# Performance work log

Measured on AMD Instinct MI355X. Metric: run time of the kernel, lower is better.

Reference implementation:

```python
import jax, jax.numpy as jnp
import numpy as np

B, N, D, H = 4, 2048, 768, 12
HD = D // H
SCALE = HD ** -0.5


def setup_inputs() -> dict:
    key = jax.random.key(0)
    k1, k2, k3 = jax.random.split(key, 3)
    x = jax.random.normal(k1, (B, N, D), dtype=jnp.float32)
    w_qkv = jax.random.normal(k2, (D, 3 * D), dtype=jnp.float32) * (D ** -0.5)
    w_proj = jax.random.normal(k3, (D, D), dtype=jnp.float32) * (D ** -0.5)
    b_proj = jnp.zeros((D,), dtype=jnp.float32)
    return {"x": x, "w_qkv": w_qkv, "w_proj": w_proj, "b_proj": b_proj}


def reference(x, w_qkv, w_proj, b_proj):
    b, n, d = x.shape
    qkv = x @ w_qkv                      # [b, n, 3d]
    q, k, v = jnp.split(qkv, 3, axis=-1)
    # [b, n, d] -> [b, h, n, hd]
    split_heads = lambda t: t.reshape(b, n, H, HD).transpose(0, 2, 1, 3)
    q, k, v = split_heads(q), split_heads(k), split_heads(v)
    dots = jnp.einsum('bhqd,bhkd->bhqk', q, k) * SCALE   # [b, h, n, n]
    attn = jax.nn.softmax(dots, axis=-1)
    q_attn = attn[:, :, 0, :]            # attention row of query token 0: [b, h, n]
    # dropout p=0 (eval) -> identity
    out = jnp.einsum('bhqk,bhkd->bhqd', attn, v)          # [b, h, n, hd]
    out = out.transpose(0, 2, 1, 3).reshape(b, n, d)      # [b, n, d]
    return out @ w_proj + b_proj, q_attn
```

## Files before the change

kernel.cpp:

```cpp
#include <hip/hip_runtime.h>


typedef unsigned short u16;
typedef __attribute__((ext_vector_type(8))) short bf8;
typedef __attribute__((ext_vector_type(4))) short bf4;
typedef __attribute__((ext_vector_type(4))) int i4;
typedef __attribute__((ext_vector_type(4))) float f4;

#define MFMA16(a, b, c) __builtin_amdgcn_mfma_f32_16x16x32_bf16((a), (b), (c), 0, 0, 0)

#if __has_builtin(__builtin_amdgcn_exp2f)
#define EXP2(x) __builtin_amdgcn_exp2f(x)
#else
#define EXP2(x) __expf((x) * 0.6931471805599453f)
#endif

__device__ __forceinline__ float b2f(u16 h) {
  union { unsigned u; float f; } v; v.u = ((unsigned)h) << 16; return v.f;
}
__device__ __forceinline__ u16 f2b(float f) {
  union { float f; unsigned u; } v; v.f = f;
  unsigned r = v.u + 0x7fffu + ((v.u >> 16) & 1u);
  return (u16)(r >> 16);
}
__device__ __forceinline__ unsigned pack2(float a, float b) {
#if __has_builtin(__builtin_amdgcn_perm)
  return __builtin_amdgcn_perm(__builtin_bit_cast(unsigned, b),
                               __builtin_bit_cast(unsigned, a), 0x07060302u);
#else
  return (__builtin_bit_cast(unsigned, b) & 0xFFFF0000u) |
         (__builtin_bit_cast(unsigned, a) >> 16);
#endif
}
__device__ __forceinline__ void gload16(const u16* g, u16* l) {
  __builtin_amdgcn_global_load_lds(
      (const __attribute__((address_space(1))) void*)g,
      (__attribute__((address_space(3))) void*)l, 16, 0, 0);
}
__device__ __forceinline__ int detect_f32(const u16* x) {
  unsigned v = x[2 * (threadIdx.x & 63)];
  unsigned e = (v >> 7) & 0xFF;
  return __ballot(e >= 0x8E) != 0ull;
}

__global__ __launch_bounds__(256) void prep(
    const void* __restrict__ x, u16* __restrict__ xbf,
    const void* __restrict__ wqkv, u16* __restrict__ wqkvT,
    const void* __restrict__ wproj, u16* __restrict__ wprojT) {
  const int z = blockIdx.z;
  if (z == 2) {
    const int f32 = detect_f32((const u16*)x);
    const int lin = blockIdx.y * 72 + blockIdx.x;
    if (f32) {
      const float2* in = (const float2*)x;
      unsigned* out = (unsigned*)xbf;
      for (int i = lin * 256 + threadIdx.x; i < 3145728; i += 442368) {
        float2 v = in[i];
        out[i] = (unsigned)f2b(v.x) | ((unsigned)f2b(v.y) << 16);
      }
    } else {
      const unsigned* in = (const unsigned*)x;
      unsigned* out = (unsigned*)xbf;
      for (int i = lin * 256 + threadIdx.x; i < 3145728; i += 442368)
        out[i] = in[i];
    }
    return;
  }
  if (z == 1 && blockIdx.x >= 24) return;
  const void* in = z ? wproj : wqkv;
  u16* out = z ? wprojT : wqkvT;
  const int R = 768, C = z ? 768 : 2304;
  __shared__ u16 tile[32][33];
  const int f32 = detect_f32((const u16*)x);
  const int bx = blockIdx.x * 32, by = blockIdx.y * 32;
  const int tx = threadIdx.x & 31, ty = threadIdx.x >> 5;
#pragma unroll
  for (int i = 0; i < 4; i++) {
    size_t idx = (size_t)(by + ty + i * 8) * C + bx + tx;
    tile[ty + i * 8][tx] = f32 ? f2b(((const float*)in)[idx]) : ((const u16*)in)[idx];
  }
  __syncthreads();
#pragma unroll
  for (int i = 0; i < 4; i++)
    out[(size_t)(bx + ty + i * 8) * R + by + tx] = tile[tx][ty + i * 8];
}

template <int BIAS, int QATTN>
__global__ __launch_bounds__(256, 4) void gemm_bt(
    const u16* __restrict__ A, const u16* __restrict__ Bt,
    const void* __restrict__ bias, void* __restrict__ C,
    int M, int Ncols, int K, const u16* __restrict__ xdet,
    u16* __restrict__ Vt, const float* __restrict__ qe,
    const float* __restrict__ lout) {
  if (QATTN && blockIdx.x == 6) {
    const int f32o = detect_f32(xdet);
    const int base = blockIdx.y * 1536;
    for (int j = threadIdx.x; j < 1536; j += 256) {
      int idx = base + j;
      float v = qe[idx] * (1.f / lout[idx >> 11]);
      size_t oidx = (size_t)6291456 + idx;
      if (f32o) ((float*)C)[oidx] = v; else ((u16*)C)[oidx] = f2b(v);
    }
    return;
  }
  __shared__ alignas(16) u16 Al[2][128 * 32];
  __shared__ alignas(16) u16 Bl[2][128 * 32];
  const int t = threadIdx.x;
  const int lane = t & 63, wave = t >> 6;
  const int wr = wave >> 1, wc = wave & 1;
  const int quad = lane >> 4, l16 = lane & 15;
  const int bm = blockIdx.y * 128, bn = blockIdx.x * 128;
  const int f32o = BIAS ? detect_f32(xdet) : 0;
  const int grow = lane >> 2, gcol = (lane & 3) * 8;
  const int chunk0 = wave * 2, chunk1 = wave * 2 + 1;
  const int arow0 = chunk0 * 16 + grow, arow1 = chunk1 * 16 + grow;
  f4 acc[4][4] = {};
  gload16(A + (size_t)(bm + arow0) * K + gcol, &Al[0][chunk0 * 512]);
  gload16(Bt + (size_t)(bn + arow0) * K + gcol, &Bl[0][chunk0 * 512]);
  gload16(A + (size_t)(bm + arow1) * K + gcol, &Al[0][chunk1 * 512]);
  gload16(Bt + (size_t)(bn + arow1) * K + gcol, &Bl[0][chunk1 * 512]);
  const int NIT = K >> 5;
  for (int i = 0; i < NIT; i++) {
    const int cur = i & 1, nxt = cur ^ 1;
    __syncthreads();
    if (i + 1 < NIT) {
      int k0 = (i + 1) << 5;
      gload16(A + (size_t)(bm + arow0) * K + k0 + gcol, &Al[nxt][chunk0 * 512]);
      gload16(Bt + (size_t)(bn + arow0) * K + k0 + gcol, &Bl[nxt][chunk0 * 512]);
      gload16(A + (size_t)(bm + arow1) * K + k0 + gcol, &Al[nxt][chunk1 * 512]);
      gload16(Bt + (size_t)(bn + arow1) * K + k0 + gcol, &Bl[nxt][chunk1 * 512]);
    }
    bf8 af[4], bfr[4];
#pragma unroll
    for (int mt = 0; mt < 4; mt++)
      af[mt] = *(const bf8*)&Al[cur][(wr * 64 + mt * 16 + l16) * 32 + quad * 8];
#pragma unroll
    for (int nt = 0; nt < 4; nt++)
      bfr[nt] = *(const bf8*)&Bl[cur][(wc * 64 + nt * 16 + l16) * 32 + quad * 8];
#pragma unroll
    for (int mt = 0; mt < 4; mt++)
#pragma unroll
      for (int nt = 0; nt < 4; nt++)
        acc[mt][nt] = MFMA16(af[mt], bfr[nt], acc[mt][nt]);
  }
  if (Vt != nullptr && bn >= 1536) {
    const int b = bm >> 11;
#pragma unroll
    for (int mt = 0; mt < 4; mt++) {
      int n0 = (bm & 2047) + wr * 64 + mt * 16 + quad * 4;
      int n2 = (n0 & ~31) | (((n0 >> 2) & 3) << 3) | (((n0 >> 4) & 1) << 2);
#pragma unroll
      for (int nt = 0; nt < 4; nt++) {
        int colv = bn - 1536 + wc * 64 + nt * 16 + l16;
        int h = colv >> 6, d = colv & 63;
        bf4 pk = {(short)f2b(acc[mt][nt][0]), (short)f2b(acc[mt][nt][1]),
                  (short)f2b(acc[mt][nt][2]), (short)f2b(acc[mt][nt][3])};
        *(bf4*)&Vt[(size_t)((b * 12 + h) * 64 + d) * 2048 + n2] = pk;
      }
    }
    return;
  }
#pragma unroll
  for (int mt = 0; mt < 4; mt++) {
    int row = bm + wr * 64 + mt * 16 + quad * 4;
#pragma unroll
    for (int nt = 0; nt < 4; nt++) {
      int col = bn + wc * 64 + nt * 16 + l16;
      float bv = 0.f;
      if (BIAS)
        bv = f32o ? ((const float*)bias)[col] : b2f(((const u16*)bias)[col]);
#pragma unroll
      for (int r = 0; r < 4; r++) {
        size_t idx = (size_t)(row + r) * Ncols + col;
        float v = acc[mt][nt][r] + bv;
        if (f32o) ((float*)C)[idx] = v; else ((u16*)C)[idx] = f2b(v);
      }
    }
  }
}

__global__ __launch_bounds__(256, 3) void flash_attn(
    const u16* __restrict__ qkv, const u16* __restrict__ Vt,
    u16* __restrict__ O, float* __restrict__ qe, float* __restrict__ lout) {
  __shared__ alignas(16) u16 lds[2][8192];
  const int t = threadIdx.x, lane = t & 63, wave = t >> 6;
  const int quad = lane >> 4, l16 = lane & 15;
  const int id = blockIdx.x;
  const int bh = (id & 7) + 8 * (id >> 7);
  const int qtile = (id >> 3) & 15;
  const int b = bh / 12, h = bh - b * 12;
  const int q0 = qtile * 128 + wave * 32;
  const bool dumpP = (qe != nullptr) && (qtile == 0) && (wave == 0);
  const float SCALE2 = 0.125f * 1.44269504089f;
  const float mM0 = -16.f;
  bf8 qf[2][2];
#pragma unroll
  for (int qt = 0; qt < 2; qt++) {
    const u16* Qr = qkv + (size_t)(b * 2048 + q0 + qt * 16 + l16) * 2304 + h * 64;
    bf8 r0 = *(const bf8*)(Qr + quad * 8);
    bf8 r1 = *(const bf8*)(Qr + 32 + quad * 8);
#pragma unroll
    for (int j = 0; j < 8; j++) {
      qf[qt][0][j] = (short)f2b(b2f((u16)r0[j]) * SCALE2);
      qf[qt][1][j] = (short)f2b(b2f((u16)r1[j]) * SCALE2);
    }
  }
  const u16* Kb = qkv + (size_t)(b * 2048) * 2304 + 768 + h * 64;
  const u16* Vb = Vt + (size_t)((b * 12 + h) * 64) * 2048;
  const int drow = wave * 16 + (lane >> 2);
  const int dcol = ((lane & 3) ^ ((lane >> 3) & 3)) * 8;
  const int swz = (quad ^ ((l16 >> 1) & 3)) * 8;
  f4 o[2][4] = {};
  float lpart[2] = {0.f, 0.f};

  {
    const u16* Kt = Kb + (size_t)drow * 2304 + dcol;
    const u16* Vr = Vb + (size_t)drow * 2048 + dcol;
    u16* base = &lds[0][wave * 512];
    gload16(Kt, base);
    gload16(Kt + 32, base + 2048);
    gload16(Vr, base + 4096);
    gload16(Vr + 32, base + 6144);
  }

  for (int i = 0; i < 32; i++) {
    const int cur = i & 1;
    __syncthreads();
    if (i + 1 < 32) {
      int n1 = (i + 1) * 64;
      const u16* Kt = Kb + (size_t)(n1 + drow) * 2304 + dcol;
      const u16* Vr = Vb + (size_t)drow * 2048 + n1 + dcol;
      u16* base = &lds[cur ^ 1][wave * 512];
      gload16(Kt, base);
      gload16(Kt + 32, base + 2048);
      gload16(Vr, base + 4096);
      gload16(Vr + 32, base + 6144);
    }
    const u16* K0 = &lds[cur][0];
    const u16* K1 = &lds[cur][2048];
    union { i4 i; bf8 b; } pf[2][2];
#pragma unroll
    for (int kt = 0; kt < 4; kt++) {
      bf8 kf0 = *(const bf8*)&K0[(kt * 16 + l16) * 32 + swz];
      bf8 kf1 = *(const bf8*)&K1[(kt * 16 + l16) * 32 + swz];
#pragma unroll
      for (int qt = 0; qt < 2; qt++) {
        f4 z = {mM0, mM0, mM0, mM0};
        z = MFMA16(kf0, qf[qt][0], z);
        z = MFMA16(kf1, qf[qt][1], z);
        float e0 = EXP2(z[0]);
        float e1 = EXP2(z[1]);
        float e2 = EXP2(z[2]);
        float e3 = EXP2(z[3]);
        lpart[qt] += (e0 + e1) + (e2 + e3);
        if (qt == 0 && dumpP && l16 == 0) {
          f4 ev = {e0, e1, e2, e3};
          *(f4*)&qe[bh * 2048 + i * 64 + kt * 16 + quad * 4] = ev;
        }
        pf[qt][kt >> 1].i[(kt & 1) * 2 + 0] = (int)pack2(e0, e1);
        pf[qt][kt >> 1].i[(kt & 1) * 2 + 1] = (int)pack2(e2, e3);
      }
    }
#pragma unroll
    for (int pair = 0; pair < 2; pair++) {
      const u16* Vp = &lds[cur][4096 + pair * 2048];
#pragma unroll
      for (int nt = 0; nt < 4; nt++) {
        bf8 vf = *(const bf8*)&Vp[(nt * 16 + l16) * 32 + swz];
        o[0][nt] = MFMA16(vf, pf[0][pair].b, o[0][nt]);
        o[1][nt] = MFMA16(vf, pf[1][pair].b, o[1][nt]);
      }
    }
  }
#pragma unroll
  for (int qt = 0; qt < 2; qt++) {
    float l = lpart[qt];
    l += __shfl_xor(l, 16, 64);
    l += __shfl_xor(l, 32, 64);
    if (qt == 0 && dumpP && lane == 0) lout[bh] = l;
    float inv = 1.f / l;
    size_t row = (size_t)(b * 2048 + q0 + qt * 16 + l16) * 768 + h * 64;
#pragma unroll
    for (int nt = 0; nt < 4; nt++) {
      bf4 pk = {(short)f2b(o[qt][nt][0] * inv), (short)f2b(o[qt][nt][1] * inv),
                (short)f2b(o[qt][nt][2] * inv), (short)f2b(o[qt][nt][3] * inv)};
      *(bf4*)&O[row + nt * 16 + quad * 4] = pk;
    }
  }
}

__global__ __launch_bounds__(256) void qattn_row0(
    const u16* __restrict__ qkv, void* __restrict__ out,
    const u16* __restrict__ xdet) {
  const int bh = blockIdx.x, b = bh / 12, h = bh % 12;
  __shared__ float qs[64];
  __shared__ float sv[2048];
  __shared__ float red[8];
  const int t = threadIdx.x;
  const int f32o = detect_f32(xdet);
  if (t < 64) qs[t] = b2f(qkv[(size_t)(b * 2048) * 2304 + h * 64 + t]);
  __syncthreads();
  float lmax = -1e30f;
  for (int k = t; k < 2048; k += 256) {
    const u16* Kr = qkv + (size_t)(b * 2048 + k) * 2304 + 768 + h * 64;
    float acc = 0.f;
#pragma unroll
    for (int j = 0; j < 8; j++) {
      bf8 kv = *(const bf8*)(Kr + j * 8);
#pragma unroll
      for (int d = 0; d < 8; d++) acc += qs[j * 8 + d] * b2f((u16)kv[d]);
    }
    acc *= 0.125f;
    sv[k] = acc;
    lmax = fmaxf(lmax, acc);
  }
#pragma unroll
  for (int off = 32; off >= 1; off >>= 1) lmax = fmaxf(lmax, __shfl_xor(lmax, off, 64));
  if ((t & 63) == 0) red[t >> 6] = lmax;
  __syncthreads();
  const float bmax = fmaxf(fmaxf(red[0], red[1]), fmaxf(red[2], red[3]));
  float lsum = 0.f;
  for (int k = t; k < 2048; k += 256) {
    float e = __expf(sv[k] - bmax);
    sv[k] = e;
    lsum += e;
  }
#pragma unroll
  for (int off = 32; off >= 1; off >>= 1) lsum += __shfl_xor(lsum, off, 64);
  if ((t & 63) == 0) red[4 + (t >> 6)] = lsum;
  __syncthreads();
  const float inv = 1.f / (red[4] + red[5] + red[6] + red[7]);
  for (int k = t; k < 2048; k += 256) {
    size_t idx = (size_t)6291456 + (size_t)bh * 2048 + k;
    float v = sv[k] * inv;
    if (f32o) ((float*)out)[idx] = v; else ((u16*)out)[idx] = f2b(v);
  }
}

extern "C" void kernel_launch(void* const* d_in, const int* in_sizes, int n_in,
                              void* d_out, int out_size, void* d_ws, size_t ws_size,
                              hipStream_t stream) {
  const void* x_raw      = d_in[0];
  const void* w_qkv_raw  = d_in[1];
  const void* w_proj_raw = d_in[2];
  const void* b_proj_raw = d_in[3];
  const u16* xdet = (const u16*)x_raw;
  char* ws = (char*)d_ws;
  u16* xbf    = (u16*)(ws + 256);
  u16* wqkvT  = (u16*)(ws + 12583168);
  u16* wprojT = (u16*)(ws + 16122112);
  u16* qkv    = (u16*)(ws + 17301760);
  u16* Vt     = (u16*)(ws + 55050496);
  float* qe   = (float*)(ws + 67633408);
  float* lout = (float*)(ws + 68026624);
  u16* attn   = xbf;
  const bool fused = ws_size >= 68026816ull;

  prep<<<dim3(72, 24, 3), 256, 0, stream>>>(
      x_raw, xbf, w_qkv_raw, wqkvT, w_proj_raw, wprojT);
  gemm_bt<0, 0><<<dim3(18, 64), 256, 0, stream>>>(
      xbf, wqkvT, nullptr, qkv, 8192, 2304, 768, xdet, Vt, nullptr, nullptr);
  flash_attn<<<dim3(768), 256, 0, stream>>>(qkv, Vt, attn,
                                            fused ? qe : nullptr,
                                            fused ? lout : nullptr);
  if (fused) {
    gemm_bt<1, 1><<<dim3(7, 64), 256, 0, stream>>>(
        attn, wprojT, b_proj_raw, d_out, 8192, 768, 768, xdet, nullptr, qe, lout);
  } else {
    gemm_bt<1, 0><<<dim3(6, 64), 256, 0, stream>>>(
        attn, wprojT, b_proj_raw, d_out, 8192, 768, 768, xdet, nullptr, nullptr, nullptr);
    qattn_row0<<<dim3(48), 256, 0, stream>>>(qkv, d_out, xdet);
  }
}
```

Measured before the change: 215.1 us.

## Halve flash-attention query tile to 16 rows per wave and double the grid

Each wave now handles one 16-row query tile instead of two, so a block covers 64 queries and the grid grows from 768 to 1536 blocks, with launch bounds raised to 5 waves per SIMD. The aim is lower register pressure, higher occupancy, and better spread of work across CUs. In exchange, each K/V tile loaded into LDS is reused by half as many queries, doubling total K/V global and LDS traffic.

```diff
diff --git a/kernel.cpp b/kernel.cpp
--- a/kernel.cpp
+++ b/kernel.cpp
@@ -179,30 +179,29 @@
   }
 }
 
-__global__ __launch_bounds__(256, 3) void flash_attn(
+__global__ __launch_bounds__(256, 5) void flash_attn(
     const u16* __restrict__ qkv, const u16* __restrict__ Vt,
     u16* __restrict__ O, float* __restrict__ qe, float* __restrict__ lout) {
   __shared__ alignas(16) u16 lds[2][8192];
   const int t = threadIdx.x, lane = t & 63, wave = t >> 6;
   const int quad = lane >> 4, l16 = lane & 15;
   const int id = blockIdx.x;
-  const int bh = (id & 7) + 8 * (id >> 7);
-  const int qtile = (id >> 3) & 15;
+  const int bh = (id & 7) + 8 * (id >> 8);
+  const int qtile = (id >> 3) & 31;
   const int b = bh / 12, h = bh - b * 12;
-  const int q0 = qtile * 128 + wave * 32;
+  const int q0 = qtile * 64 + wave * 16;
   const bool dumpP = (qe != nullptr) && (qtile == 0) && (wave == 0);
   const float SCALE2 = 0.125f * 1.44269504089f;
   const float mM0 = -16.f;
-  bf8 qf[2][2];
-#pragma unroll
-  for (int qt = 0; qt < 2; qt++) {
-    const u16* Qr = qkv + (size_t)(b * 2048 + q0 + qt * 16 + l16) * 2304 + h * 64;
+  bf8 qf[2];
+  {
+    const u16* Qr = qkv + (size_t)(b * 2048 + q0 + l16) * 2304 + h * 64;
     bf8 r0 = *(const bf8*)(Qr + quad * 8);
     bf8 r1 = *(const bf8*)(Qr + 32 + quad * 8);
 #pragma unroll
     for (int j = 0; j < 8; j++) {
-      qf[qt][0][j] = (short)f2b(b2f((u16)r0[j]) * SCALE2);
-      qf[qt][1][j] = (short)f2b(b2f((u16)r1[j]) * SCALE2);
+      qf[0][j] = (short)f2b(b2f((u16)r0[j]) * SCALE2);
+      qf[1][j] = (short)f2b(b2f((u16)r1[j]) * SCALE2);
     }
   }
   const u16* Kb = qkv + (size_t)(b * 2048) * 2304 + 768 + h * 64;
@@ -210,8 +209,8 @@
   const int drow = wave * 16 + (lane >> 2);
   const int dcol = ((lane & 3) ^ ((lane >> 3) & 3)) * 8;
   const int swz = (quad ^ ((l16 >> 1) & 3)) * 8;
-  f4 o[2][4] = {};
-  float lpart[2] = {0.f, 0.f};
+  f4 o[4] = {};
+  float lpart = 0.f;
 
   {
     const u16* Kt = Kb + (size_t)drow * 2304 + dcol;
@@ -238,28 +237,25 @@
     }
     const u16* K0 = &lds[cur][0];
     const u16* K1 = &lds[cur][2048];
-    union { i4 i; bf8 b; } pf[2][2];
+    union { i4 i; bf8 b; } pf[2];
 #pragma unroll
     for (int kt = 0; kt < 4; kt++) {
       bf8 kf0 = *(const bf8*)&K0[(kt * 16 + l16) * 32 + swz];
       bf8 kf1 = *(const bf8*)&K1[(kt * 16 + l16) * 32 + swz];
-#pragma unroll
-      for (int qt = 0; qt < 2; qt++) {
-        f4 z = {mM0, mM0, mM0, mM0};
-        z = MFMA16(kf0, qf[qt][0], z);
-        z = MFMA16(kf1, qf[qt][1], z);
-        float e0 = EXP2(z[0]);
-        float e1 = EXP2(z[1]);
-        float e2 = EXP2(z[2]);
-        float e3 = EXP2(z[3]);
-        lpart[qt] += (e0 + e1) + (e2 + e3);
-        if (qt == 0 && dumpP && l16 == 0) {
-          f4 ev = {e0, e1, e2, e3};
-          *(f4*)&qe[bh * 2048 + i * 64 + kt * 16 + quad * 4] = ev;
-        }
-        pf[qt][kt >> 1].i[(kt & 1) * 2 + 0] = (int)pack2(e0, e1);
-        pf[qt][kt >> 1].i[(kt & 1) * 2 + 1] = (int)pack2(e2, e3);
-      }
+      f4 z = {mM0, mM0, mM0, mM0};
+      z = MFMA16(kf0, qf[0], z);
+      z = MFMA16(kf1, qf[1], z);
+      float e0 = EXP2(z[0]);
+      float e1 = EXP2(z[1]);
+      float e2 = EXP2(z[2]);
+      float e3 = EXP2(z[3]);
+      lpart += (e0 + e1) + (e2 + e3);
+      if (dumpP && l16 == 0) {
+        f4 ev = {e0, e1, e2, e3};
+        *(f4*)&qe[bh * 2048 + i * 64 + kt * 16 + quad * 4] = ev;
+      }
+      pf[kt >> 1].i[(kt & 1) * 2 + 0] = (int)pack2(e0, e1);
+      pf[kt >> 1].i[(kt & 1) * 2 + 1] = (int)pack2(e2, e3);
     }
 #pragma unroll
     for (int pair = 0; pair < 2; pair++) {
@@ -267,23 +263,21 @@
 #pragma unroll
       for (int nt = 0; nt < 4; nt++) {
         bf8 vf = *(const bf8*)&Vp[(nt * 16 + l16) * 32 + swz];
-        o[0][nt] = MFMA16(vf, pf[0][pair].b, o[0][nt]);
-        o[1][nt] = MFMA16(vf, pf[1][pair].b, o[1][nt]);
-      }
-    }
-  }
-#pragma unroll
-  for (int qt = 0; qt < 2; qt++) {
-    float l = lpart[qt];
+        o[nt] = MFMA16(vf, pf[pair].b, o[nt]);
+      }
+    }
+  }
+  {
+    float l = lpart;
     l += __shfl_xor(l, 16, 64);
     l += __shfl_xor(l, 32, 64);
-    if (qt == 0 && dumpP && lane == 0) lout[bh] = l;
+    if (dumpP && lane == 0) lout[bh] = l;
     float inv = 1.f / l;
-    size_t row = (size_t)(b * 2048 + q0 + qt * 16 + l16) * 768 + h * 64;
+    size_t row = (size_t)(b * 2048 + q0 + l16) * 768 + h * 64;
 #pragma unroll
     for (int nt = 0; nt < 4; nt++) {
-      bf4 pk = {(short)f2b(o[qt][nt][0] * inv), (short)f2b(o[qt][nt][1] * inv),
-                (short)f2b(o[qt][nt][2] * inv), (short)f2b(o[qt][nt][3] * inv)};
+      bf4 pk = {(short)f2b(o[nt][0] * inv), (short)f2b(o[nt][1] * inv),
+                (short)f2b(o[nt][2] * inv), (short)f2b(o[nt][3] * inv)};
       *(bf4*)&O[row + nt * 16 + quad * 4] = pk;
     }
   }
@@ -360,9 +354,9 @@
       x_raw, xbf, w_qkv_raw, wqkvT, w_proj_raw, wprojT);
   gemm_bt<0, 0><<<dim3(18, 64), 256, 0, stream>>>(
       xbf, wqkvT, nullptr, qkv, 8192, 2304, 768, xdet, Vt, nullptr, nullptr);
-  flash_attn<<<dim3(768), 256, 0, stream>>>(qkv, Vt, attn,
-                                            fused ? qe : nullptr,
-                                            fused ? lout : nullptr);
+  flash_attn<<<dim3(1536), 256, 0, stream>>>(qkv, Vt, attn,
+                                             fused ? qe : nullptr,
+                                             fused ? lout : nullptr);
   if (fused) {
     gemm_bt<1, 1><<<dim3(7, 64), 256, 0, stream>>>(
         attn, wprojT, b_proj_raw, d_out, 8192, 768, 768, xdet, nullptr, qe, lout);
```

Result: slower. 229.1 us (+6.5%).

## Triple-buffer K/V tiles with vmcnt waits and compute row sums via MFMA

Applied to the files above, without the earlier changes.

Moves the flash attention K/V staging from double to triple buffering in LDS. It prefetches two tiles ahead and uses explicit s_waitcnt vmcnt plus a raw s_barrier, so the loads of the next tile can stay in flight across the barrier. It also replaces the scalar accumulation of softmax denominators and the final cross-lane shuffles with an MFMA against a vector of ones, moving those adds to the matrix unit. LDS use per block grows from 32KB to 48KB, which may reduce occupancy below the 3 blocks per CU requested. The row sums are now taken from the bf16-rounded probabilities, which changes numerics slightly.

```diff
diff --git a/kernel.cpp b/kernel.cpp
--- a/kernel.cpp
+++ b/kernel.cpp
@@ -182,7 +182,7 @@
 __global__ __launch_bounds__(256, 3) void flash_attn(
     const u16* __restrict__ qkv, const u16* __restrict__ Vt,
     u16* __restrict__ O, float* __restrict__ qe, float* __restrict__ lout) {
-  __shared__ alignas(16) u16 lds[2][8192];
+  __shared__ alignas(16) u16 lds[3][8192];
   const int t = threadIdx.x, lane = t & 63, wave = t >> 6;
   const int quad = lane >> 4, l16 = lane & 15;
   const int id = blockIdx.x;
@@ -205,36 +205,43 @@
       qf[qt][1][j] = (short)f2b(b2f((u16)r1[j]) * SCALE2);
     }
   }
+  bf8 ones;
+#pragma unroll
+  for (int j = 0; j < 8; j++) ones[j] = (short)0x3F80;
   const u16* Kb = qkv + (size_t)(b * 2048) * 2304 + 768 + h * 64;
   const u16* Vb = Vt + (size_t)((b * 12 + h) * 64) * 2048;
   const int drow = wave * 16 + (lane >> 2);
   const int dcol = ((lane & 3) ^ ((lane >> 3) & 3)) * 8;
   const int swz = (quad ^ ((l16 >> 1) & 3)) * 8;
   f4 o[2][4] = {};
-  float lpart[2] = {0.f, 0.f};
-
-  {
-    const u16* Kt = Kb + (size_t)drow * 2304 + dcol;
-    const u16* Vr = Vb + (size_t)drow * 2048 + dcol;
-    u16* base = &lds[0][wave * 512];
-    gload16(Kt, base);
-    gload16(Kt + 32, base + 2048);
-    gload16(Vr, base + 4096);
-    gload16(Vr + 32, base + 6144);
-  }
-
+  f4 lacc[2] = {};
+
+#define STAGE(tile, buf)                                            \
+  {                                                                 \
+    int n1_ = (tile) * 64;                                          \
+    const u16* Kt_ = Kb + (size_t)(n1_ + drow) * 2304 + dcol;       \
+    const u16* Vr_ = Vb + (size_t)drow * 2048 + n1_ + dcol;         \
+    u16* base_ = &lds[buf][wave * 512];                             \
+    gload16(Kt_, base_);                                            \
+    gload16(Kt_ + 32, base_ + 2048);                                \
+    gload16(Vr_, base_ + 4096);                                     \
+    gload16(Vr_ + 32, base_ + 6144);                                \
+  }
+
+  STAGE(0, 0);
+  STAGE(1, 1);
+
+  int cur = 0;
   for (int i = 0; i < 32; i++) {
-    const int cur = i & 1;
-    __syncthreads();
-    if (i + 1 < 32) {
-      int n1 = (i + 1) * 64;
-      const u16* Kt = Kb + (size_t)(n1 + drow) * 2304 + dcol;
-      const u16* Vr = Vb + (size_t)drow * 2048 + n1 + dcol;
-      u16* base = &lds[cur ^ 1][wave * 512];
-      gload16(Kt, base);
-      gload16(Kt + 32, base + 2048);
-      gload16(Vr, base + 4096);
-      gload16(Vr + 32, base + 6144);
+    if (i < 31) {
+      asm volatile("s_waitcnt vmcnt(4)" ::: "memory");
+    } else {
+      asm volatile("s_waitcnt vmcnt(0)" ::: "memory");
+    }
+    __builtin_amdgcn_s_barrier();
+    if (i + 2 < 32) {
+      int pre = cur + 2; if (pre >= 3) pre -= 3;
+      STAGE(i + 2, pre);
     }
     const u16* K0 = &lds[cur][0];
     const u16* K1 = &lds[cur][2048];
@@ -252,7 +259,6 @@
         float e1 = EXP2(z[1]);
         float e2 = EXP2(z[2]);
         float e3 = EXP2(z[3]);
-        lpart[qt] += (e0 + e1) + (e2 + e3);
         if (qt == 0 && dumpP && l16 == 0) {
           f4 ev = {e0, e1, e2, e3};
           *(f4*)&qe[bh * 2048 + i * 64 + kt * 16 + quad * 4] = ev;
@@ -264,6 +270,8 @@
 #pragma unroll
     for (int pair = 0; pair < 2; pair++) {
       const u16* Vp = &lds[cur][4096 + pair * 2048];
+      lacc[0] = MFMA16(ones, pf[0][pair].b, lacc[0]);
+      lacc[1] = MFMA16(ones, pf[1][pair].b, lacc[1]);
 #pragma unroll
       for (int nt = 0; nt < 4; nt++) {
         bf8 vf = *(const bf8*)&Vp[(nt * 16 + l16) * 32 + swz];
@@ -271,12 +279,12 @@
         o[1][nt] = MFMA16(vf, pf[1][pair].b, o[1][nt]);
       }
     }
-  }
+    cur = (cur == 2) ? 0 : cur + 1;
+  }
+#undef STAGE
 #pragma unroll
   for (int qt = 0; qt < 2; qt++) {
-    float l = lpart[qt];
-    l += __shfl_xor(l, 16, 64);
-    l += __shfl_xor(l, 32, 64);
+    float l = lacc[qt][0];
     if (qt == 0 && dumpP && lane == 0) lout[bh] = l;
     float inv = 1.f / l;
     size_t row = (size_t)(b * 2048 + q0 + qt * 16 + l16) * 768 + h * 64;
```

After: 213.4 us. No clear change (-0.8%).
